# Kernel tuning notes

Hardware: AMD Instinct MI355X
Metric: run time of the kernel (lower is better)

The kernel has to match this reference:

```python
import jax, jax.numpy as jnp
import numpy as np

B, I, H, OH = 16384, 256, 256, 64
N_STEPS = 8  # fixed-step dopri5 (adaptive step control replaced by fixed grid for jit)


def setup_inputs() -> dict:
    key = jax.random.key(0)
    ks = jax.random.split(key, 12)
    sH = 1.0 / np.sqrt(H)
    sOH = 1.0 / np.sqrt(OH)
    u = lambda k, shape, s: jax.random.uniform(k, shape, jnp.float32, -s, s)
    return {
        "input": jax.random.normal(ks[0], (B, I), jnp.float32),
        "h_prev": jax.random.normal(ks[1], (B, H), jnp.float32),
        "c_prev": jax.random.normal(ks[2], (B, H), jnp.float32),
        "timespans": jax.random.uniform(ks[3], (B,), jnp.float32, 0.05, 1.0),
        # LSTMCell params (PyTorch layout: gates stacked as [i, f, g, o])
        "W_ih": u(ks[4], (4 * H, I), sH),
        "W_hh": u(ks[5], (4 * H, H), sH),
        "b_ih": u(ks[6], (4 * H,), sH),
        "b_hh": u(ks[7], (4 * H,), sH),
        # ode_func: Linear(H, OH) -> Tanh -> Linear(OH, H)
        "W1": u(ks[8], (OH, H), sH),
        "b1": u(ks[9], (OH,), sH),
        "W2": u(ks[10], (H, OH), sOH),
        "b2": u(ks[11], (H,), sOH),
    }


def reference(input, h_prev, c_prev, timespans, W_ih, W_hh, b_ih, b_hh, W1, b1, W2, b2):
    # --- LSTMCell ---
    gates = input @ W_ih.T + b_ih + h_prev @ W_hh.T + b_hh  # (B, 4H)
    gi, gf, gg, go = jnp.split(gates, 4, axis=-1)
    i = jax.nn.sigmoid(gi)
    f = jax.nn.sigmoid(gf)
    g = jnp.tanh(gg)
    o = jax.nn.sigmoid(go)
    c = f * c_prev + i * g
    h = o * jnp.tanh(c)

    # --- Neural ODE: dy/dt = MLP(y), autonomous, Dormand-Prince RK45 ---
    def ode_f(y):
        return jnp.tanh(y @ W1.T + b1) @ W2.T + b2

    dt = (timespans / N_STEPS)[:, None]  # (B, 1) per-sample step size

    def dopri5_step(y, _):
        k1 = ode_f(y)
        k2 = ode_f(y + dt * (1.0 / 5.0 * k1))
        k3 = ode_f(y + dt * (3.0 / 40.0 * k1 + 9.0 / 40.0 * k2))
        k4 = ode_f(y + dt * (44.0 / 45.0 * k1 - 56.0 / 15.0 * k2 + 32.0 / 9.0 * k3))
        k5 = ode_f(y + dt * (19372.0 / 6561.0 * k1 - 25360.0 / 2187.0 * k2
                             + 64448.0 / 6561.0 * k3 - 212.0 / 729.0 * k4))
        k6 = ode_f(y + dt * (9017.0 / 3168.0 * k1 - 355.0 / 33.0 * k2
                             + 46732.0 / 5247.0 * k3 + 49.0 / 176.0 * k4
                             - 5103.0 / 18656.0 * k5))
        y_next = y + dt * (35.0 / 384.0 * k1 + 500.0 / 1113.0 * k3 + 125.0 / 192.0 * k4
                           - 2187.0 / 6784.0 * k5 + 11.0 / 84.0 * k6)
        return y_next, None

    h_ode, _ = jax.lax.scan(dopri5_step, h, None, length=N_STEPS)
    return h_ode, c
```

## Files before the change

kernel.cpp:

```cpp
#include <hip/hip_runtime.h>
#include <hip/hip_bf16.h>


#define B_N 16384
#define H_N 256

typedef __attribute__((ext_vector_type(8))) short short8;
typedef __attribute__((ext_vector_type(4))) unsigned short u16x4;
typedef __attribute__((ext_vector_type(4))) float f32x4;

__device__ __forceinline__ unsigned short f2bf_s(float x) {
  __hip_bfloat16 h = __float2bfloat16(x);
  return *reinterpret_cast<unsigned short*>(&h);
}

__device__ __forceinline__ short8 pack8f(const float* p) {
  const f32x4 a = *(const f32x4*)p;
  const f32x4 b = *(const f32x4*)(p + 4);
  short8 r;
  r[0] = (short)f2bf_s(a[0]); r[1] = (short)f2bf_s(a[1]);
  r[2] = (short)f2bf_s(a[2]); r[3] = (short)f2bf_s(a[3]);
  r[4] = (short)f2bf_s(b[0]); r[5] = (short)f2bf_s(b[1]);
  r[6] = (short)f2bf_s(b[2]); r[7] = (short)f2bf_s(b[3]);
  return r;
}

__device__ __forceinline__ short8 pack8v(f32x4 a, f32x4 b) {
  short8 r;
  r[0] = (short)f2bf_s(a[0]); r[1] = (short)f2bf_s(a[1]);
  r[2] = (short)f2bf_s(a[2]); r[3] = (short)f2bf_s(a[3]);
  r[4] = (short)f2bf_s(b[0]); r[5] = (short)f2bf_s(b[1]);
  r[6] = (short)f2bf_s(b[2]); r[7] = (short)f2bf_s(b[3]);
  return r;
}

__device__ __forceinline__ float fast_sigmoid(float x) {
  return __builtin_amdgcn_rcpf(1.f + __expf(-x));
}
__device__ __forceinline__ float fast_tanh(float x) {
  float e = __expf(2.f * x);
  return 1.f - 2.f * __builtin_amdgcn_rcpf(e + 1.f);
}

__device__ __forceinline__ void gl_lds16(const void* g, void* l) {
  __builtin_amdgcn_global_load_lds(
      (const __attribute__((address_space(1))) void*)g,
      (__attribute__((address_space(3))) void*)l, 16, 0, 0);
}

__global__ __launch_bounds__(256) void prep_kernel(
    const float* __restrict__ Wih, const float* __restrict__ Whh,
    const float* __restrict__ W1, const float* __restrict__ W2,
    const float* __restrict__ b2,
    unsigned short* __restrict__ wsB, unsigned short* __restrict__ wcB,
    float* __restrict__ uF, unsigned short* __restrict__ w1B,
    unsigned short* __restrict__ w2B) {
  const int bx = blockIdx.x;
  if (bx < 256) {
    int idx = bx * 256 + threadIdx.x;
    int n = idx >> 6, c = idx & 63, k = c * 8;
    const float* src = (k < 256) ? (Wih + (size_t)n * 256 + k)
                                 : (Whh + (size_t)n * 256 + (k - 256));
    *(short8*)(wsB + (size_t)n * 512 + k) = pack8f(src);
  } else if (bx < 272) {
    int idx = (bx - 256) * 256 + threadIdx.x;
    int f = idx >> 6, o = idx & 63;
    float a0 = 0.f, a1 = 0.f, a2 = 0.f, a3 = 0.f;
    for (int h = 0; h < 256; h += 4) {
      a0 = fmaf(W1[f * 256 + h],     W2[h * 64 + o],        a0);
      a1 = fmaf(W1[f * 256 + h + 1], W2[(h + 1) * 64 + o],  a1);
      a2 = fmaf(W1[f * 256 + h + 2], W2[(h + 2) * 64 + o],  a2);
      a3 = fmaf(W1[f * 256 + h + 3], W2[(h + 3) * 64 + o],  a3);
    }
    wcB[f * 64 + o] = f2bf_s((a0 + a1) + (a2 + a3));
  } else if (bx == 272) {
    int f = threadIdx.x;
    if (f < 64) {
      float a0 = 0.f, a1 = 0.f, a2 = 0.f, a3 = 0.f;
      for (int h = 0; h < 256; h += 4) {
        a0 = fmaf(W1[f * 256 + h],     b2[h],     a0);
        a1 = fmaf(W1[f * 256 + h + 1], b2[h + 1], a1);
        a2 = fmaf(W1[f * 256 + h + 2], b2[h + 2], a2);
        a3 = fmaf(W1[f * 256 + h + 3], b2[h + 3], a3);
      }
      uF[f] = (a0 + a1) + (a2 + a3);
    }
  } else if (bx < 281) {
    int idx = (bx - 273) * 256 + threadIdx.x;
    *(short8*)(w1B + (size_t)idx * 8) = pack8f(W1 + (size_t)idx * 8);
  } else {
    int idx = (bx - 281) * 256 + threadIdx.x;
    *(short8*)(w2B + (size_t)idx * 8) = pack8f(W2 + (size_t)idx * 8);
  }
}

__global__ __launch_bounds__(512, 4) void lstm_kernel(
    const float* __restrict__ x, const float* __restrict__ hp,
    const float* __restrict__ cp, const unsigned short* __restrict__ wsB,
    const float* __restrict__ bih, const float* __restrict__ bhh,
    float* __restrict__ out) {
  __shared__ __align__(16) float As2[2][128 * 32];
  __shared__ __align__(16) unsigned short Bs2[2][256 * 32];

  const int tid = threadIdx.x;
  const int lane = tid & 63;
  const int wv = tid >> 6;
  const int rg = wv >> 1;
  const int cg = wv & 1;
  const int s = lane & 15, q = lane >> 4;
  const int mb = blockIdx.x * 128;
  const int hb = blockIdx.y * 64;

  f32x4 acc[2][8];
#pragma unroll
  for (int mt = 0; mt < 2; ++mt)
#pragma unroll
    for (int tn = 0; tn < 8; ++tn) acc[mt][tn] = (f32x4){0.f, 0.f, 0.f, 0.f};

  const int c16a = wv * 2;
  const int rowA0 = c16a * 8 + (lane >> 3);
  const int gcA = (lane & 7) ^ (rowA0 & 7);
  const int rowB0 = c16a * 16 + (lane >> 2);
  const int rowB1 = rowB0 + 16;
  const int gcB0 = (lane & 3) ^ ((rowB0 >> 1) & 3);
  const int gcB1 = (lane & 3) ^ ((rowB1 >> 1) & 3);
  const int grB0 = (rowB0 >> 6) * 256 + hb + (rowB0 & 63);
  const int grB1 = (rowB1 >> 6) * 256 + hb + (rowB1 & 63);

  auto STAGE = [&](int buf, int kt) {
    const float* srcA = (kt < 8) ? x : hp;
    const int kl = (kt * 32) & 255;
    gl_lds16(srcA + (size_t)(mb + rowA0) * 256 + kl + gcA * 4,
             (char*)As2[buf] + c16a * 1024);
    gl_lds16(srcA + (size_t)(mb + rowA0 + 8) * 256 + kl + gcA * 4,
             (char*)As2[buf] + (c16a + 1) * 1024);
    gl_lds16(wsB + (size_t)grB0 * 512 + kt * 32 + gcB0 * 8,
             (char*)Bs2[buf] + c16a * 1024);
    gl_lds16(wsB + (size_t)grB1 * 512 + kt * 32 + gcB1 * 8,
             (char*)Bs2[buf] + (c16a + 1) * 1024);
  };

  STAGE(0, 0);
  __syncthreads();

  for (int kt = 0; kt < 16; ++kt) {
    const int buf = kt & 1;
    if (kt < 15) STAGE(buf ^ 1, kt + 1);

    short8 af[2];
#pragma unroll
    for (int mt = 0; mt < 2; ++mt) {
      const int ar = rg * 32 + mt * 16 + s;
      const char* ap = (const char*)As2[buf] + ar * 128;
      float tmp[8];
      *(f32x4*)tmp = *(const f32x4*)(ap + (((q * 2) ^ (ar & 7)) << 4));
      *(f32x4*)(tmp + 4) = *(const f32x4*)(ap + (((q * 2 + 1) ^ (ar & 7)) << 4));
      af[mt] = pack8f(tmp);
    }
    const char* bp = (const char*)Bs2[buf];
#pragma unroll
    for (int tn = 0; tn < 8; ++tn) {
      const int t = (tn >> 1) * 64 + cg * 32 + (tn & 1) * 16 + s;
      short8 bfr = *(const short8*)(bp + t * 64 + ((q ^ ((t >> 1) & 3)) << 4));
      acc[0][tn] = __builtin_amdgcn_mfma_f32_16x16x32_bf16(af[0], bfr, acc[0][tn], 0, 0, 0);
      acc[1][tn] = __builtin_amdgcn_mfma_f32_16x16x32_bf16(af[1], bfr, acc[1][tn], 0, 0, 0);
    }
    __syncthreads();
  }

#pragma unroll
  for (int mt = 0; mt < 2; ++mt)
#pragma unroll
    for (int ntl = 0; ntl < 2; ++ntl)
#pragma unroll
      for (int r = 0; r < 4; ++r) {
        int sample = mb + rg * 32 + mt * 16 + q * 4 + r;
        int h = hb + cg * 32 + ntl * 16 + s;
        float gi = acc[mt][0 + ntl][r] + bih[h] + bhh[h];
        float gf = acc[mt][2 + ntl][r] + bih[256 + h] + bhh[256 + h];
        float gg = acc[mt][4 + ntl][r] + bih[512 + h] + bhh[512 + h];
        float go = acc[mt][6 + ntl][r] + bih[768 + h] + bhh[768 + h];
        float iv = fast_sigmoid(gi), fv = fast_sigmoid(gf);
        float gv = fast_tanh(gg), ov = fast_sigmoid(go);
        float c = fv * cp[(size_t)sample * 256 + h] + iv * gv;
        float hv = ov * fast_tanh(c);
        out[(size_t)B_N * H_N + (size_t)sample * 256 + h] = c;
        out[(size_t)sample * 256 + h] = hv;
      }
}

__global__ __launch_bounds__(64) void ode_kernel(
    float* __restrict__ out, const float* __restrict__ ts,
    const unsigned short* __restrict__ wcB, const float* __restrict__ uF,
    const unsigned short* __restrict__ w1B, const unsigned short* __restrict__ w2B,
    const float* __restrict__ b1, const float* __restrict__ b2) {
  const int lane = threadIdx.x;
  const int s = lane & 15, q = lane >> 4;
  const int bb = blockIdx.x * 16;

  auto grow = [&](int i) {
    return (i >> 1) * 32 + ((s >> 2) * 8) + (i & 1) * 4 + (s & 3);
  };
  auto fbase = [&](int i) { return (i >> 1) * 32 + q * 8 + (i & 1) * 4; };

  short8 wcf[4][2];
#pragma unroll
  for (int i = 0; i < 4; ++i) {
    const int gr = grow(i);
#pragma unroll
    for (int kt = 0; kt < 2; ++kt)
      wcf[i][kt] = *(const short8*)(wcB + (size_t)gr * 64 + kt * 32 + q * 8);
  }
  f32x4 b1v[4], u4[4];
#pragma unroll
  for (int i = 0; i < 4; ++i) {
    b1v[i] = *(const f32x4*)(b1 + fbase(i));
    u4[i] = *(const f32x4*)(uF + fbase(i));
  }
  const float dt = ts[bb + s] * 0.125f;

  f32x4 G[4];
#pragma unroll
  for (int i = 0; i < 4; ++i) G[i] = (f32x4){0.f, 0.f, 0.f, 0.f};
#pragma unroll
  for (int kt = 0; kt < 8; ++kt) {
    short8 yf = pack8f(out + (size_t)(bb + s) * 256 + kt * 32 + q * 8);
#pragma unroll
    for (int i = 0; i < 4; ++i) {
      short8 w1f =
          *(const short8*)(w1B + (size_t)grow(i) * 256 + kt * 32 + q * 8);
      G[i] = __builtin_amdgcn_mfma_f32_16x16x32_bf16(w1f, yf, G[i], 0, 0, 0);
    }
  }

  auto wcmm = [&](const f32x4 (&zc)[4], f32x4 (&o)[4]) {
    short8 zf0 = pack8v(zc[0], zc[1]);
    short8 zf1 = pack8v(zc[2], zc[3]);
#pragma unroll
    for (int i = 0; i < 4; ++i) {
      f32x4 a = (f32x4){0.f, 0.f, 0.f, 0.f};
      a = __builtin_amdgcn_mfma_f32_16x16x32_bf16(wcf[i][0], zf0, a, 0, 0, 0);
      a = __builtin_amdgcn_mfma_f32_16x16x32_bf16(wcf[i][1], zf1, a, 0, 0, 0);
      o[i] = a;
    }
  };
  auto stage = [&](const f32x4 (&zc)[4], float cj, f32x4 (&zo)[4]) {
    f32x4 o[4];
    wcmm(zc, o);
#pragma unroll
    for (int i = 0; i < 4; ++i)
#pragma unroll
      for (int r = 0; r < 4; ++r)
        zo[i][r] =
            fast_tanh(fmaf(dt, fmaf(cj, u4[i][r], o[i][r]), G[i][r]) + b1v[i][r]);
  };

  const float A31 = 3.f / 40.f, A32 = 9.f / 40.f;
  const float A41 = 44.f / 45.f, A42 = -56.f / 15.f, A43 = 32.f / 9.f;
  const float A51 = 19372.f / 6561.f, A52 = -25360.f / 2187.f,
              A53 = 64448.f / 6561.f, A54 = -212.f / 729.f;
  const float A61 = 9017.f / 3168.f, A62 = -355.f / 33.f, A63 = 46732.f / 5247.f,
              A64 = 49.f / 176.f, A65 = -5103.f / 18656.f;
  const float C1 = 35.f / 384.f, C3 = 500.f / 1113.f, C4 = 125.f / 192.f,
              C5 = -2187.f / 6784.f, C6 = 11.f / 84.f;

  f32x4 SC[4];
#pragma unroll
  for (int i = 0; i < 4; ++i) SC[i] = (f32x4){0.f, 0.f, 0.f, 0.f};
  f32x4 z1[4], z2[4], z3[4], z4[4], z5[4], zc[4];

  for (int st = 0; st < 8; ++st) {
#pragma unroll
    for (int i = 0; i < 4; ++i)
#pragma unroll
      for (int r = 0; r < 4; ++r) z1[i][r] = fast_tanh(G[i][r] + b1v[i][r]);

#pragma unroll
    for (int i = 0; i < 4; ++i) zc[i] = 0.2f * z1[i];
    stage(zc, 0.2f, z2);
#pragma unroll
    for (int i = 0; i < 4; ++i) zc[i] = A31 * z1[i] + A32 * z2[i];
    stage(zc, 0.3f, z3);
#pragma unroll
    for (int i = 0; i < 4; ++i) zc[i] = A41 * z1[i] + A42 * z2[i] + A43 * z3[i];
    stage(zc, 0.8f, z4);
#pragma unroll
    for (int i = 0; i < 4; ++i)
      zc[i] = A51 * z1[i] + A52 * z2[i] + A53 * z3[i] + A54 * z4[i];
    stage(zc, 8.f / 9.f, z5);
#pragma unroll
    for (int i = 0; i < 4; ++i)
      zc[i] = A61 * z1[i] + A62 * z2[i] + A63 * z3[i] + A64 * z4[i] + A65 * z5[i];
    {
      f32x4 o[4];
      wcmm(zc, o);
#pragma unroll
      for (int i = 0; i < 4; ++i)
#pragma unroll
        for (int r = 0; r < 4; ++r) {
          float z6v =
              fast_tanh(fmaf(dt, u4[i][r] + o[i][r], G[i][r]) + b1v[i][r]);
          zc[i][r] = C1 * z1[i][r] + C3 * z3[i][r] + C4 * z4[i][r] +
                     C5 * z5[i][r] + C6 * z6v;
        }
    }
    {
      f32x4 o6[4];
      wcmm(zc, o6);
#pragma unroll
      for (int i = 0; i < 4; ++i) {
        SC[i] += zc[i];
#pragma unroll
        for (int r = 0; r < 4; ++r)
          G[i][r] = fmaf(dt, u4[i][r] + o6[i][r], G[i][r]);
      }
    }
  }

  {
    short8 sf0 = pack8v(SC[0], SC[1]);
    short8 sf1 = pack8v(SC[2], SC[3]);
#pragma unroll
    for (int ft = 0; ft < 16; ++ft) {
      short8 w2a = *(const short8*)(w2B + (size_t)(ft * 16 + s) * 64 + q * 8);
      short8 w2b = *(const short8*)(w2B + (size_t)(ft * 16 + s) * 64 + 32 + q * 8);
      f32x4 a = (f32x4){0.f, 0.f, 0.f, 0.f};
      a = __builtin_amdgcn_mfma_f32_16x16x32_bf16(w2a, sf0, a, 0, 0, 0);
      a = __builtin_amdgcn_mfma_f32_16x16x32_bf16(w2b, sf1, a, 0, 0, 0);
      f32x4 y0 = *(const f32x4*)(out + (size_t)(bb + s) * 256 + ft * 16 + q * 4);
      f32x4 b2v = *(const f32x4*)(b2 + ft * 16 + q * 4);
#pragma unroll
      for (int r = 0; r < 4; ++r)
        y0[r] = fmaf(dt, fmaf(8.f, b2v[r], a[r]), y0[r]);
      *(f32x4*)(out + (size_t)(bb + s) * 256 + ft * 16 + q * 4) = y0;
    }
  }
}

extern "C" void kernel_launch(void* const* d_in, const int* in_sizes, int n_in,
                              void* d_out, int out_size, void* d_ws, size_t ws_size,
                              hipStream_t stream) {
  const float* x   = (const float*)d_in[0];
  const float* hp  = (const float*)d_in[1];
  const float* cp  = (const float*)d_in[2];
  const float* ts  = (const float*)d_in[3];
  const float* Wih = (const float*)d_in[4];
  const float* Whh = (const float*)d_in[5];
  const float* bih = (const float*)d_in[6];
  const float* bhh = (const float*)d_in[7];
  const float* W1  = (const float*)d_in[8];
  const float* b1  = (const float*)d_in[9];
  const float* W2  = (const float*)d_in[10];
  const float* b2  = (const float*)d_in[11];
  float* out = (float*)d_out;

  unsigned short* wsB = (unsigned short*)d_ws;
  unsigned short* wcB = (unsigned short*)((char*)d_ws + 1048576);
  float* uF = (float*)((char*)d_ws + 1048576 + 8192);
  unsigned short* w1B = (unsigned short*)((char*)d_ws + 1048576 + 16384);
  unsigned short* w2B = (unsigned short*)((char*)d_ws + 1048576 + 49152);

  prep_kernel<<<289, 256, 0, stream>>>(Wih, Whh, W1, W2, b2, wsB, wcB, uF, w1B, w2B);
  lstm_kernel<<<dim3(128, 4), 512, 0, stream>>>(x, hp, cp, wsB, bih, bhh, out);
  ode_kernel<<<1024, 64, 0, stream>>>(out, ts, wcB, uF, w1B, w2B, b1, b2);
}
```

Before: 80.73 us.

## Pipeline LSTM GEMM loads with vmcnt waits and fold b1 into ODE state

Rewrites the LSTM gate GEMM main loop so each iteration issues the next tile's global-to-LDS loads, waits on vmcnt(4) plus a raw s_barrier, computes the current tile, and peels off the final tile. This replaces the per-iteration __syncthreads with a partial wait meant to overlap loads with MFMA work. Separately, the b1 bias is added into G once before the ODE loop instead of inside every tanh evaluation. Two unused lambdas (COMPUTE, COMPUTE8) are left behind as dead code, and the manual waitcnt depends on the exact number of loads issued per STAGE.

```diff
diff --git a/kernel.cpp b/kernel.cpp
--- a/kernel.cpp
+++ b/kernel.cpp
@@ -140,13 +140,53 @@
              (char*)Bs2[buf] + (c16a + 1) * 1024);
   };
 
-  STAGE(0, 0);
-  __syncthreads();
-
-  for (int kt = 0; kt < 16; ++kt) {
-    const int buf = kt & 1;
-    if (kt < 15) STAGE(buf ^ 1, kt + 1);
-
+  auto COMPUTE = [&](int buf) {
+#pragma unroll
+    for (int kk = 0; kk < 2; ++kk) {
+      short8 af[2];
+#pragma unroll
+      for (int mt = 0; mt < 2; ++mt) {
+        const int ar = rg * 32 + mt * 16 + s;
+        const char* ap = (const char*)As2[buf] + ar * 128;
+        float tmp[8];
+        *(f32x4*)tmp = *(const f32x4*)(ap + (((kk * 8 + q * 2) ^ (ar & 7)) << 4) -
+                                       (kk * 8 ^ 0) * 0);
+        af[mt] = af[mt];
+      }
+    }
+  };
+  (void)0;
+
+  auto COMPUTE8 = [&](int buf) {
+#pragma unroll
+    for (int kk = 0; kk < 2; ++kk) {
+      short8 af[2];
+#pragma unroll
+      for (int mt = 0; mt < 2; ++mt) {
+        const int ar = rg * 32 + mt * 16 + s;
+        const char* ap = (const char*)As2[buf] + ar * 128;
+        float tmp[8];
+        *(f32x4*)tmp = *(const f32x4*)(ap + (((q * 2) ^ (ar & 7)) << 4));
+        *(f32x4*)(tmp + 4) =
+            *(const f32x4*)(ap + (((q * 2 + 1) ^ (ar & 7)) << 4));
+        af[mt] = pack8f(tmp);
+      }
+      const char* bp = (const char*)Bs2[buf];
+#pragma unroll
+      for (int tn = 0; tn < 8; ++tn) {
+        const int t = (tn >> 1) * 64 + cg * 32 + (tn & 1) * 16 + s;
+        short8 bfr = *(const short8*)(bp + t * 64 + ((q ^ ((t >> 1) & 3)) << 4));
+        acc[0][tn] =
+            __builtin_amdgcn_mfma_f32_16x16x32_bf16(af[0], bfr, acc[0][tn], 0, 0, 0);
+        acc[1][tn] =
+            __builtin_amdgcn_mfma_f32_16x16x32_bf16(af[1], bfr, acc[1][tn], 0, 0, 0);
+      }
+      if (kk == 0) continue;
+    }
+  };
+  (void)0;
+
+  auto COMPUTE32 = [&](int buf) {
     short8 af[2];
 #pragma unroll
     for (int mt = 0; mt < 2; ++mt) {
@@ -162,11 +202,28 @@
     for (int tn = 0; tn < 8; ++tn) {
       const int t = (tn >> 1) * 64 + cg * 32 + (tn & 1) * 16 + s;
       short8 bfr = *(const short8*)(bp + t * 64 + ((q ^ ((t >> 1) & 3)) << 4));
-      acc[0][tn] = __builtin_amdgcn_mfma_f32_16x16x32_bf16(af[0], bfr, acc[0][tn], 0, 0, 0);
-      acc[1][tn] = __builtin_amdgcn_mfma_f32_16x16x32_bf16(af[1], bfr, acc[1][tn], 0, 0, 0);
-    }
-    __syncthreads();
-  }
+      acc[0][tn] =
+          __builtin_amdgcn_mfma_f32_16x16x32_bf16(af[0], bfr, acc[0][tn], 0, 0, 0);
+      acc[1][tn] =
+          __builtin_amdgcn_mfma_f32_16x16x32_bf16(af[1], bfr, acc[1][tn], 0, 0, 0);
+    }
+  };
+
+  STAGE(0, 0);
+#pragma unroll 1
+  for (int kt = 0; kt < 15; ++kt) {
+    const int buf = kt & 1;
+    STAGE(buf ^ 1, kt + 1);
+    asm volatile("s_waitcnt vmcnt(4)" ::: "memory");
+    __builtin_amdgcn_s_barrier();
+    __builtin_amdgcn_sched_barrier(0);
+    COMPUTE32(buf);
+    __builtin_amdgcn_s_barrier();
+  }
+  asm volatile("s_waitcnt vmcnt(0)" ::: "memory");
+  __builtin_amdgcn_s_barrier();
+  __builtin_amdgcn_sched_barrier(0);
+  COMPUTE32(1);
 
 #pragma unroll
   for (int mt = 0; mt < 2; ++mt)
@@ -232,6 +289,8 @@
       G[i] = __builtin_amdgcn_mfma_f32_16x16x32_bf16(w1f, yf, G[i], 0, 0, 0);
     }
   }
+#pragma unroll
+  for (int i = 0; i < 4; ++i) G[i] += b1v[i];
 
   auto wcmm = [&](const f32x4 (&zc)[4], f32x4 (&o)[4]) {
     short8 zf0 = pack8v(zc[0], zc[1]);
@@ -251,8 +310,7 @@
     for (int i = 0; i < 4; ++i)
 #pragma unroll
       for (int r = 0; r < 4; ++r)
-        zo[i][r] =
-            fast_tanh(fmaf(dt, fmaf(cj, u4[i][r], o[i][r]), G[i][r]) + b1v[i][r]);
+        zo[i][r] = fast_tanh(fmaf(dt, fmaf(cj, u4[i][r], o[i][r]), G[i][r]));
   };
 
   const float A31 = 3.f / 40.f, A32 = 9.f / 40.f;
@@ -273,7 +331,7 @@
 #pragma unroll
     for (int i = 0; i < 4; ++i)
 #pragma unroll
-      for (int r = 0; r < 4; ++r) z1[i][r] = fast_tanh(G[i][r] + b1v[i][r]);
+      for (int r = 0; r < 4; ++r) z1[i][r] = fast_tanh(G[i][r]);
 
 #pragma unroll
     for (int i = 0; i < 4; ++i) zc[i] = 0.2f * z1[i];
@@ -298,8 +356,7 @@
       for (int i = 0; i < 4; ++i)
 #pragma unroll
         for (int r = 0; r < 4; ++r) {
-          float z6v =
-              fast_tanh(fmaf(dt, u4[i][r] + o[i][r], G[i][r]) + b1v[i][r]);
+          float z6v = fast_tanh(fmaf(dt, u4[i][r] + o[i][r], G[i][r]));
           zc[i][r] = C1 * z1[i][r] + C3 * z3[i][r] + C4 * z4[i][r] +
                      C5 * z5[i][r] + C6 * z6v;
         }
```

Result: faster. 78.48 us (-2.8%).
